# Kernel optimization log

Measured on AMD Instinct MI355X. Metric: run time of the kernel, lower is better.

Reference implementation:

```python
import jax, jax.numpy as jnp
import numpy as np

B, L_TEXT, N_TOKEN = 8, 2048, 2048
C_TEXT, C_OUT = 3584, 384
C_HID = C_OUT * 2
CHAIN_TYPES = (1, 2)   # heavy, light
CDR_TYPES = (2, 4, 6)  # CDR1/2/3


def setup_inputs() -> dict:
    key = jax.random.key(0)
    ks = jax.random.split(key, 10)
    text_conditioning = jax.random.normal(ks[0], (B, L_TEXT, C_TEXT), jnp.float32)
    text_mask = jnp.ones((B, L_TEXT), jnp.int32)
    chain_type_ids = jax.random.randint(ks[1], (B, L_TEXT), 0, 3).astype(jnp.int32)
    cdr_region_type_ids = jax.random.randint(ks[2], (B, L_TEXT), 0, 10).astype(jnp.int32)
    boltz_chain_type = jax.random.randint(ks[3], (B, N_TOKEN), 0, 4).astype(jnp.int32)
    boltz_region_type = jax.random.randint(ks[4], (B, N_TOKEN), 0, 10).astype(jnp.int32)
    W1 = jax.random.normal(ks[5], (C_HID, C_TEXT), jnp.float32) * 0.02
    b1 = jnp.zeros((C_HID,), jnp.float32)
    W2 = jax.random.normal(ks[6], (C_OUT, C_HID), jnp.float32) * 0.02
    b2 = jnp.zeros((C_OUT,), jnp.float32)
    scale = jnp.ones((1,), jnp.float32)
    return {
        "text_conditioning": text_conditioning, "text_mask": text_mask,
        "chain_type_ids": chain_type_ids, "cdr_region_type_ids": cdr_region_type_ids,
        "boltz_chain_type": boltz_chain_type, "boltz_region_type": boltz_region_type,
        "W1": W1, "b1": b1, "W2": W2, "b2": b2, "scale": scale,
    }


def _align_one(text_proj, tmask, pmask):
    # text_proj: [L, C]; tmask: [L] bool (text CDR positions); pmask: [N] bool (protein CDR positions)
    # The k-th masked text token (in sequence order) maps to the k-th masked protein token,
    # for k < min(n_text, n_protein). Other protein positions get zeros.
    L = tmask.shape[0]
    trank = jnp.cumsum(tmask) - 1          # rank among text CDR tokens
    n_text = jnp.sum(tmask)
    prank = jnp.cumsum(pmask) - 1          # rank among protein CDR tokens
    # idx_by_rank[r] = text index whose rank is r; out-of-range scatter indices dropped
    idx_by_rank = jnp.zeros((L,), jnp.int32).at[jnp.where(tmask, trank, L)].set(
        jnp.arange(L, dtype=jnp.int32), mode="drop")
    valid = pmask & (prank < n_text)       # prank < n_protein holds by construction under pmask
    src = idx_by_rank[jnp.clip(prank, 0, L - 1)]
    emb = text_proj[src]                   # [N, C]
    return jnp.where(valid[:, None], emb, jnp.zeros((), text_proj.dtype))


def reference(text_conditioning, text_mask, chain_type_ids, cdr_region_type_ids,
              boltz_chain_type, boltz_region_type, W1, b1, W2, b2, scale):
    # 2-layer MLP projection: c_text -> 2*c_out -> c_out with SiLU
    h = jax.nn.silu(jnp.einsum("blt,ht->blh", text_conditioning, W1) + b1)
    text_proj = jnp.einsum("blh,ch->blc", h, W2) + b2    # [B, L, C_OUT]

    tm = text_mask.astype(bool)
    result = jnp.zeros((text_conditioning.shape[0], boltz_chain_type.shape[1], W2.shape[0]),
                       text_proj.dtype)
    align = jax.vmap(_align_one)
    for ct in CHAIN_TYPES:
        for rt in CDR_TYPES:
            tmask = (chain_type_ids == ct) & (cdr_region_type_ids == rt) & tm
            pmask = (boltz_chain_type == ct) & (boltz_region_type == rt)
            # (chain, cdr) pairs write to disjoint protein positions, so add is exact
            result = result + align(text_proj, tmask, pmask)
    return scale * result
```

## Files before the change

### kernel.cpp

```cpp
#include <hip/hip_runtime.h>
#include <hip/hip_bf16.h>
#include <math.h>

typedef __bf16 bf16_t;
typedef bf16_t bf16x8 __attribute__((ext_vector_type(8)));
typedef bf16_t bf16x4 __attribute__((ext_vector_type(4)));
typedef float f32x4 __attribute__((ext_vector_type(4)));

#define L_TEXT 2048
#define N_TOKEN 2048
#define C_TEXT 3584
#define C_OUT 384
#define C_HID 768
#define BATCH 8
#define MAXROWS (BATCH * N_TOKEN)
#define PM 3072
#define NPAIR (BATCH * 6)
#define KSPLIT 4
#define KCHUNK (C_TEXT / KSPLIT)
#define KSPLIT2 2
#define KCHUNK2 (C_HID / KSPLIT2)

#define NW1 (C_HID * C_TEXT / 8)
#define NW2 (C_OUT * C_HID / 8)
#define NINV (MAXROWS / 4)
#define CVT_BLOCKS ((NW1 + NW2 + NINV) / 256)
#define GCH (C_TEXT / 8)

__global__ __launch_bounds__(256) void init_map_kernel(
    const float* __restrict__ W1, const float* __restrict__ W2,
    bf16_t* __restrict__ W1b, bf16_t* __restrict__ W2b,
    int* __restrict__ inv,
    const int* __restrict__ tm, const int* __restrict__ ctid,
    const int* __restrict__ cdrid, const int* __restrict__ bct,
    const int* __restrict__ brt,
    int* __restrict__ trowL, int* __restrict__ pidxL, int* __restrict__ vcnt) {
    if (blockIdx.x >= CVT_BLOCKS) {
        const int bp = blockIdx.x - CVT_BLOCKS;
        const int lane = threadIdx.x;
        if (lane >= 64) return;
        const int b = bp / 6, p = bp % 6;
        const int ct = (p < 3) ? 1 : 2;
        const int rt = 2 + 2 * (p % 3);
        const unsigned long long ltm = (1ull << lane) - 1ull;

        unsigned int tbits = 0, pbits = 0;
#pragma unroll
        for (int i = 0; i < 32; i++) {
            int l = i * 64 + lane;
            unsigned int m = (ctid[b * L_TEXT + l] == ct) &&
                             (cdrid[b * L_TEXT + l] == rt) &&
                             (tm[b * L_TEXT + l] != 0);
            tbits |= m << i;
        }
#pragma unroll
        for (int i = 0; i < 32; i++) {
            int n = i * 64 + lane;
            unsigned int m = (bct[b * N_TOKEN + n] == ct) &&
                             (brt[b * N_TOKEN + n] == rt);
            pbits |= m << i;
        }

        int base = 0;
#pragma unroll
        for (int i = 0; i < 32; i++) {
            bool m = (tbits >> i) & 1;
            unsigned long long bal = __ballot(m);
            if (m) trowL[bp * L_TEXT + base + __popcll(bal & ltm)] = i * 64 + lane;
            base += __popcll(bal);
        }
        const int n_text = base;

        base = 0;
#pragma unroll
        for (int i = 0; i < 32; i++) {
            bool m = (pbits >> i) & 1;
            unsigned long long bal = __ballot(m);
            if (m) pidxL[bp * L_TEXT + base + __popcll(bal & ltm)] = i * 64 + lane;
            base += __popcll(bal);
        }
        const int n_prot = base;
        if (lane == 0) vcnt[bp] = n_text < n_prot ? n_text : n_prot;
        return;
    }

    int idx = blockIdx.x * 256 + threadIdx.x;
    if (idx < NW1) {
        int i = idx * 8;
        float4 v0 = *(const float4*)(W1 + i);
        float4 v1 = *(const float4*)(W1 + i + 4);
        bf16x8 o;
        o[0] = (bf16_t)v0.x; o[1] = (bf16_t)v0.y; o[2] = (bf16_t)v0.z; o[3] = (bf16_t)v0.w;
        o[4] = (bf16_t)v1.x; o[5] = (bf16_t)v1.y; o[6] = (bf16_t)v1.z; o[7] = (bf16_t)v1.w;
        *(bf16x8*)(W1b + i) = o;
    } else if (idx < NW1 + NW2) {
        int i = (idx - NW1) * 8;
        float4 v0 = *(const float4*)(W2 + i);
        float4 v1 = *(const float4*)(W2 + i + 4);
        bf16x8 o;
        o[0] = (bf16_t)v0.x; o[1] = (bf16_t)v0.y; o[2] = (bf16_t)v0.z; o[3] = (bf16_t)v0.w;
        o[4] = (bf16_t)v1.x; o[5] = (bf16_t)v1.y; o[6] = (bf16_t)v1.z; o[7] = (bf16_t)v1.w;
        *(bf16x8*)(W2b + i) = o;
    } else {
        int i = idx - NW1 - NW2;
        int4 m1 = {-1, -1, -1, -1};
        ((int4*)inv)[i] = m1;
    }
}

__global__ __launch_bounds__(64) void map_write_kernel(
    const int* __restrict__ trowL, const int* __restrict__ pidxL,
    const int* __restrict__ vcnt,
    int* __restrict__ rows_src, int* __restrict__ inv, int* __restrict__ count) {
    const int bp = blockIdx.x;
    const int b = bp / 6;
    const int lane = threadIdx.x;
    int base = 0, total = 0;
    for (int q = 0; q < NPAIR; q++) {
        int v = vcnt[q];
        if (q < bp) base += v;
        total += v;
    }
    if (bp == 0 && lane == 0) *count = total < PM ? total : PM;
    const int v = vcnt[bp];
    for (int r = lane; r < v; r += 64) {
        int g = base + r;
        if (g < PM) {
            rows_src[g] = b * L_TEXT + trowL[bp * L_TEXT + r];
            inv[b * N_TOKEN + pidxL[bp * L_TEXT + r]] = g;
        }
    }
}

__global__ __launch_bounds__(256) void gather_kernel(
    const float* __restrict__ X, const int* __restrict__ rows_src,
    const int* __restrict__ countp, bf16_t* __restrict__ Xg) {
    int count = *countp; if (count > PM) count = PM;
    int idx = blockIdx.x * 256 + threadIdx.x;
    int m = idx / GCH;
    if (m >= count) return;
    int c = (idx % GCH) * 8;
    const float* src = X + (size_t)rows_src[m] * C_TEXT + c;
    float4 v0 = *(const float4*)(src);
    float4 v1 = *(const float4*)(src + 4);
    bf16x8 o;
    o[0] = (bf16_t)v0.x; o[1] = (bf16_t)v0.y; o[2] = (bf16_t)v0.z; o[3] = (bf16_t)v0.w;
    o[4] = (bf16_t)v1.x; o[5] = (bf16_t)v1.y; o[6] = (bf16_t)v1.z; o[7] = (bf16_t)v1.w;
    *(bf16x8*)(Xg + (size_t)m * C_TEXT + c) = o;
}

__global__ __launch_bounds__(256) void gemm1_kernel(
    const bf16_t* __restrict__ Xg, const bf16_t* __restrict__ W1b,
    const int* __restrict__ countp, float* __restrict__ P) {
    int count = *countp; if (count > PM) count = PM;
    const int m0 = blockIdx.x * 128;
    if (m0 >= count) return;
    const int n0 = blockIdx.y * 128;
    const int kbeg = blockIdx.z * KCHUNK;

    __shared__ __align__(16) bf16_t As[2][128][40];
    __shared__ __align__(16) bf16_t Bs[2][128][40];

    const int t = threadIdx.x;
    const int lane = t & 63;
    const int w = t >> 6;
    const int wr = w >> 1, wc = w & 1;
    const int fr = lane & 15;
    const int kq = (lane >> 4) * 8;

    f32x4 acc[4][4];
#pragma unroll
    for (int i = 0; i < 4; i++)
#pragma unroll
        for (int j = 0; j < 4; j++) acc[i][j] = (f32x4){0.f, 0.f, 0.f, 0.f};

    const bf16_t* ap[2];
    const bf16_t* bp[2];
    int ofs[2];
#pragma unroll
    for (int j = 0; j < 2; j++) {
        int c = t + 256 * j;
        int row = c >> 2, c8 = (c & 3) * 8;
        ap[j] = Xg + (size_t)(m0 + row) * C_TEXT + kbeg + c8;
        bp[j] = W1b + (size_t)(n0 + row) * C_TEXT + kbeg + c8;
        ofs[j] = row * 40 + c8;
    }

    bf16_t* AsF = &As[0][0][0];
    bf16_t* BsF = &Bs[0][0][0];
    const int BUF = 128 * 40;

    bf16x8 ra[2], rb[2];
#pragma unroll
    for (int j = 0; j < 2; j++) { ra[j] = *(const bf16x8*)(ap[j]); rb[j] = *(const bf16x8*)(bp[j]); }

    const int T = KCHUNK / 32;
    for (int tile = 0; tile < T; ++tile) {
        const int cur = tile & 1;
#pragma unroll
        for (int j = 0; j < 2; j++) {
            *(bf16x8*)(AsF + cur * BUF + ofs[j]) = ra[j];
            *(bf16x8*)(BsF + cur * BUF + ofs[j]) = rb[j];
        }
        bf16x8 na[2], nb[2];
        bool more = (tile + 1 < T);
        if (more) {
            int k = (tile + 1) * 32;
#pragma unroll
            for (int j = 0; j < 2; j++) {
                na[j] = *(const bf16x8*)(ap[j] + k);
                nb[j] = *(const bf16x8*)(bp[j] + k);
            }
        }
        __syncthreads();
        bf16x8 af[4], bfr[4];
#pragma unroll
        for (int mi = 0; mi < 4; mi++)
            af[mi] = *(const bf16x8*)(AsF + cur * BUF + (wr * 64 + mi * 16 + fr) * 40 + kq);
#pragma unroll
        for (int ni = 0; ni < 4; ni++)
            bfr[ni] = *(const bf16x8*)(BsF + cur * BUF + (wc * 64 + ni * 16 + fr) * 40 + kq);
#pragma unroll
        for (int mi = 0; mi < 4; mi++)
#pragma unroll
            for (int ni = 0; ni < 4; ni++)
                acc[mi][ni] = __builtin_amdgcn_mfma_f32_16x16x32_bf16(
                    af[mi], bfr[ni], acc[mi][ni], 0, 0, 0);
        if (more) {
#pragma unroll
            for (int j = 0; j < 2; j++) { ra[j] = na[j]; rb[j] = nb[j]; }
        }
    }

    float* Pk = P + (size_t)blockIdx.z * PM * C_HID;
    const int rj = (lane >> 4) * 4;
#pragma unroll
    for (int mi = 0; mi < 4; mi++) {
#pragma unroll
        for (int ni = 0; ni < 4; ni++) {
            int gn = n0 + wc * 64 + ni * 16 + fr;
#pragma unroll
            for (int j = 0; j < 4; j++) {
                int gm = m0 + wr * 64 + mi * 16 + rj + j;
                if (gm < count) Pk[(size_t)gm * C_HID + gn] = acc[mi][ni][j];
            }
        }
    }
}

__global__ __launch_bounds__(256) void reduce1_kernel(
    const float* __restrict__ P, const float* __restrict__ b1,
    const int* __restrict__ countp, bf16_t* __restrict__ H) {
    int count = *countp; if (count > PM) count = PM;
    int idx = blockIdx.x * 256 + threadIdx.x;
    int m = idx / (C_HID / 4);
    int c = (idx % (C_HID / 4)) * 4;
    if (m >= count) return;
    f32x4 s = *(const f32x4*)(P + (size_t)m * C_HID + c);
#pragma unroll
    for (int ks = 1; ks < KSPLIT; ks++)
        s += *(const f32x4*)(P + ((size_t)ks * PM + m) * C_HID + c);
    f32x4 bb = *(const f32x4*)(b1 + c);
    bf16x4 o;
#pragma unroll
    for (int j = 0; j < 4; j++) {
        float v = s[j] + bb[j];
        o[j] = (bf16_t)(v / (1.0f + __expf(-v)));
    }
    *(bf16x4*)(H + (size_t)m * C_HID + c) = o;
}

__global__ __launch_bounds__(256) void gemm2_kernel(
    const bf16_t* __restrict__ Hm, const bf16_t* __restrict__ W2b,
    const int* __restrict__ countp, float* __restrict__ P2) {
    int count = *countp; if (count > PM) count = PM;
    const int m0 = blockIdx.x * 64;
    if (m0 >= count) return;
    const int n0 = blockIdx.y * 128;
    const int kbeg = blockIdx.z * KCHUNK2;

    __shared__ __align__(16) bf16_t As[2][64][40];
    __shared__ __align__(16) bf16_t Bs[2][128][40];

    const int t = threadIdx.x;
    const int lane = t & 63;
    const int w = t >> 6;
    const int wr = w >> 1, wc = w & 1;
    const int fr = lane & 15;
    const int kq = (lane >> 4) * 8;

    f32x4 acc[2][4];
#pragma unroll
    for (int i = 0; i < 2; i++)
#pragma unroll
        for (int j = 0; j < 4; j++) acc[i][j] = (f32x4){0.f, 0.f, 0.f, 0.f};

    const int arow = t >> 2, ac8 = (t & 3) * 8;
    const bf16_t* ap = Hm + (size_t)(m0 + arow) * C_HID + kbeg + ac8;
    const int aofs = arow * 40 + ac8;
    const bf16_t* bp[2];
    int bofs[2];
#pragma unroll
    for (int j = 0; j < 2; j++) {
        int c = t + 256 * j;
        int row = c >> 2, c8 = (c & 3) * 8;
        bp[j] = W2b + (size_t)(n0 + row) * C_HID + kbeg + c8;
        bofs[j] = row * 40 + c8;
    }

    bf16_t* AsF = &As[0][0][0];
    bf16_t* BsF = &Bs[0][0][0];
    const int ABUF = 64 * 40, BBUF = 128 * 40;

    bf16x8 ra = *(const bf16x8*)(ap);
    bf16x8 rb0 = *(const bf16x8*)(bp[0]);
    bf16x8 rb1 = *(const bf16x8*)(bp[1]);

    const int T = KCHUNK2 / 32;
    for (int tile = 0; tile < T; ++tile) {
        const int cur = tile & 1;
        *(bf16x8*)(AsF + cur * ABUF + aofs) = ra;
        *(bf16x8*)(BsF + cur * BBUF + bofs[0]) = rb0;
        *(bf16x8*)(BsF + cur * BBUF + bofs[1]) = rb1;
        bf16x8 na, nb0, nb1;
        bool more = (tile + 1 < T);
        if (more) {
            int k = (tile + 1) * 32;
            na = *(const bf16x8*)(ap + k);
            nb0 = *(const bf16x8*)(bp[0] + k);
            nb1 = *(const bf16x8*)(bp[1] + k);
        }
        __syncthreads();
        bf16x8 af[2], bfr[4];
#pragma unroll
        for (int mi = 0; mi < 2; mi++)
            af[mi] = *(const bf16x8*)(AsF + cur * ABUF + (wr * 32 + mi * 16 + fr) * 40 + kq);
#pragma unroll
        for (int ni = 0; ni < 4; ni++)
            bfr[ni] = *(const bf16x8*)(BsF + cur * BBUF + (wc * 64 + ni * 16 + fr) * 40 + kq);
#pragma unroll
        for (int mi = 0; mi < 2; mi++)
#pragma unroll
            for (int ni = 0; ni < 4; ni++)
                acc[mi][ni] = __builtin_amdgcn_mfma_f32_16x16x32_bf16(
                    af[mi], bfr[ni], acc[mi][ni], 0, 0, 0);
        if (more) { ra = na; rb0 = nb0; rb1 = nb1; }
    }

    float* Pk = P2 + (size_t)blockIdx.z * PM * C_OUT;
    const int rj = (lane >> 4) * 4;
#pragma unroll
    for (int mi = 0; mi < 2; mi++) {
#pragma unroll
        for (int ni = 0; ni < 4; ni++) {
            int gn = n0 + wc * 64 + ni * 16 + fr;
#pragma unroll
            for (int j = 0; j < 4; j++) {
                int gm = m0 + wr * 32 + mi * 16 + rj + j;
                if (gm < count) Pk[(size_t)gm * C_OUT + gn] = acc[mi][ni][j];
            }
        }
    }
}

__global__ __launch_bounds__(256) void out_kernel(
    const float* __restrict__ P2, const float* __restrict__ b2,
    const int* __restrict__ inv, const float* __restrict__ scale,
    float* __restrict__ out) {
    int idx = blockIdx.x * 256 + threadIdx.x;
    int token = idx / (C_OUT / 4);
    int c = (idx % (C_OUT / 4)) * 4;
    int m = inv[token];
    f32x4 o = (f32x4){0.f, 0.f, 0.f, 0.f};
    if (m >= 0) {
        f32x4 s = *(const f32x4*)(P2 + (size_t)m * C_OUT + c);
#pragma unroll
        for (int ks = 1; ks < KSPLIT2; ks++)
            s += *(const f32x4*)(P2 + ((size_t)ks * PM + m) * C_OUT + c);
        f32x4 bb = *(const f32x4*)(b2 + c);
        const float sc = scale[0];
#pragma unroll
        for (int j = 0; j < 4; j++) o[j] = sc * (s[j] + bb[j]);
    }
    *(f32x4*)(out + (size_t)token * C_OUT + c) = o;
}

extern "C" void kernel_launch(void* const* d_in, const int* in_sizes, int n_in,
                              void* d_out, int out_size, void* d_ws, size_t ws_size,
                              hipStream_t stream) {
    const float* X     = (const float*)d_in[0];
    const int*   tm    = (const int*)d_in[1];
    const int*   ctid  = (const int*)d_in[2];
    const int*   cdrid = (const int*)d_in[3];
    const int*   bct   = (const int*)d_in[4];
    const int*   brt   = (const int*)d_in[5];
    const float* W1    = (const float*)d_in[6];
    const float* b1    = (const float*)d_in[7];
    const float* W2    = (const float*)d_in[8];
    const float* b2    = (const float*)d_in[9];
    const float* scale = (const float*)d_in[10];

    char* ws = (char*)d_ws;
    size_t off = 0;
    int* count = (int*)(ws + off);        off += 1024;
    int* vcnt = (int*)(ws + off);         off += 1024;
    int* rows_src = (int*)(ws + off);     off += (size_t)PM * 4;
    int* inv = (int*)(ws + off);          off += (size_t)MAXROWS * 4;
    int* trowL = (int*)(ws + off);        off += (size_t)NPAIR * L_TEXT * 4;
    int* pidxL = (int*)(ws + off);        off += (size_t)NPAIR * L_TEXT * 4;
    bf16_t* W1b = (bf16_t*)(ws + off);    off += (size_t)C_HID * C_TEXT * 2;
    bf16_t* W2b = (bf16_t*)(ws + off);    off += (size_t)C_OUT * C_HID * 2;
    bf16_t* Xg = (bf16_t*)(ws + off);     off += (size_t)PM * C_TEXT * 2;
    bf16_t* H = (bf16_t*)(ws + off);      off += (size_t)PM * C_HID * 2;
    float* P = (float*)(ws + off);        off += (size_t)KSPLIT * PM * C_HID * 4;
    float* P2 = P;

    init_map_kernel<<<CVT_BLOCKS + NPAIR, 256, 0, stream>>>(
        W1, W2, W1b, W2b, inv, tm, ctid, cdrid, bct, brt, trowL, pidxL, vcnt);

    map_write_kernel<<<NPAIR, 64, 0, stream>>>(trowL, pidxL, vcnt,
                                               rows_src, inv, count);

    gather_kernel<<<(PM * GCH) / 256, 256, 0, stream>>>(X, rows_src, count, Xg);

    dim3 g1(PM / 128, C_HID / 128, KSPLIT);
    gemm1_kernel<<<g1, 256, 0, stream>>>(Xg, W1b, count, P);

    reduce1_kernel<<<(PM * C_HID / 4) / 256, 256, 0, stream>>>(P, b1, count, H);

    dim3 g2(PM / 64, C_OUT / 128, KSPLIT2);
    gemm2_kernel<<<g2, 256, 0, stream>>>(H, W2b, count, P2);

    out_kernel<<<(MAXROWS * C_OUT / 4) / 256, 256, 0, stream>>>(
        P2, b2, inv, scale, (float*)d_out);
}
```

Measured before the change: 126.5 us.

## Fuse all stages into one cooperative persistent kernel with grid syncs

Replaces the seven-kernel pipeline with a single cooperative kernel that runs every stage (weight conversion and mapping, row map write, GEMM1, SiLU reduce, GEMM2, output scatter) in grid-strided loops separated by grid.sync. GEMM1 now reads the gathered fp32 text rows directly and converts them to bf16 in-register, so the separate gather pass and its Xg buffer are no longer used. GEMM2 split-K goes from 2 to 4 to give more work units to the persistent grid. This removes launch overhead and one full gather round-trip, at the cost of grid-wide barriers, a fixed grid size tied to occupancy, and fp32 loads inside the GEMM inner loop. The old multi-kernel path is kept as a fallback.

```diff
diff --git a/kernel.cpp b/kernel.cpp
--- a/kernel.cpp
+++ b/kernel.cpp
@@ -1,6 +1,9 @@
 #include <hip/hip_runtime.h>
 #include <hip/hip_bf16.h>
+#include <hip/hip_cooperative_groups.h>
 #include <math.h>
+
+namespace cg = cooperative_groups;
 
 typedef __bf16 bf16_t;
 typedef bf16_t bf16x8 __attribute__((ext_vector_type(8)));
@@ -18,14 +21,378 @@
 #define NPAIR (BATCH * 6)
 #define KSPLIT 4
 #define KCHUNK (C_TEXT / KSPLIT)
-#define KSPLIT2 2
+#define KSPLIT2 4
 #define KCHUNK2 (C_HID / KSPLIT2)
+#define KSPLIT2F 2
+#define KCHUNK2F (C_HID / KSPLIT2F)
 
 #define NW1 (C_HID * C_TEXT / 8)
 #define NW2 (C_OUT * C_HID / 8)
 #define NINV (MAXROWS / 4)
 #define CVT_BLOCKS ((NW1 + NW2 + NINV) / 256)
 #define GCH (C_TEXT / 8)
+
+__global__ __launch_bounds__(256, 2) void mega_kernel(
+    const float* __restrict__ X, const int* __restrict__ tm,
+    const int* __restrict__ ctid, const int* __restrict__ cdrid,
+    const int* __restrict__ bct, const int* __restrict__ brt,
+    const float* __restrict__ W1, const float* __restrict__ b1,
+    const float* __restrict__ W2, const float* __restrict__ b2,
+    const float* __restrict__ scale,
+    bf16_t* __restrict__ W1b, bf16_t* __restrict__ W2b,
+    int* __restrict__ inv, int* __restrict__ count, int* __restrict__ vcnt,
+    int* __restrict__ rows_src, int* __restrict__ trowL, int* __restrict__ pidxL,
+    bf16_t* __restrict__ H, float* __restrict__ P, float* __restrict__ outp)
+{
+    cg::grid_group grid = cg::this_grid();
+    const int nb = gridDim.x;
+    const int t = threadIdx.x;
+
+    __shared__ __align__(16) bf16_t As[2][128][40];
+    __shared__ __align__(16) bf16_t Bs[2][128][40];
+    bf16_t* AsF = &As[0][0][0];
+    bf16_t* BsF = &Bs[0][0][0];
+
+    for (int u = blockIdx.x; u < CVT_BLOCKS + NPAIR; u += nb) {
+        if (u < CVT_BLOCKS) {
+            int idx = u * 256 + t;
+            if (idx < NW1) {
+                int i = idx * 8;
+                float4 v0 = *(const float4*)(W1 + i);
+                float4 v1 = *(const float4*)(W1 + i + 4);
+                bf16x8 o;
+                o[0] = (bf16_t)v0.x; o[1] = (bf16_t)v0.y; o[2] = (bf16_t)v0.z; o[3] = (bf16_t)v0.w;
+                o[4] = (bf16_t)v1.x; o[5] = (bf16_t)v1.y; o[6] = (bf16_t)v1.z; o[7] = (bf16_t)v1.w;
+                *(bf16x8*)(W1b + i) = o;
+            } else if (idx < NW1 + NW2) {
+                int i = (idx - NW1) * 8;
+                float4 v0 = *(const float4*)(W2 + i);
+                float4 v1 = *(const float4*)(W2 + i + 4);
+                bf16x8 o;
+                o[0] = (bf16_t)v0.x; o[1] = (bf16_t)v0.y; o[2] = (bf16_t)v0.z; o[3] = (bf16_t)v0.w;
+                o[4] = (bf16_t)v1.x; o[5] = (bf16_t)v1.y; o[6] = (bf16_t)v1.z; o[7] = (bf16_t)v1.w;
+                *(bf16x8*)(W2b + i) = o;
+            } else {
+                int i = idx - NW1 - NW2;
+                int4 m1 = {-1, -1, -1, -1};
+                ((int4*)inv)[i] = m1;
+            }
+        } else if (t < 64) {
+            const int bp = u - CVT_BLOCKS;
+            const int lane = t;
+            const int b = bp / 6, p = bp % 6;
+            const int ct = (p < 3) ? 1 : 2;
+            const int rt = 2 + 2 * (p % 3);
+            const unsigned long long ltm = (1ull << lane) - 1ull;
+
+            unsigned int tbits = 0, pbits = 0;
+#pragma unroll
+            for (int i = 0; i < 32; i++) {
+                int l = i * 64 + lane;
+                unsigned int m = (ctid[b * L_TEXT + l] == ct) &&
+                                 (cdrid[b * L_TEXT + l] == rt) &&
+                                 (tm[b * L_TEXT + l] != 0);
+                tbits |= m << i;
+            }
+#pragma unroll
+            for (int i = 0; i < 32; i++) {
+                int n = i * 64 + lane;
+                unsigned int m = (bct[b * N_TOKEN + n] == ct) &&
+                                 (brt[b * N_TOKEN + n] == rt);
+                pbits |= m << i;
+            }
+            int base = 0;
+#pragma unroll
+            for (int i = 0; i < 32; i++) {
+                bool m = (tbits >> i) & 1;
+                unsigned long long bal = __ballot(m);
+                if (m) trowL[bp * L_TEXT + base + __popcll(bal & ltm)] = i * 64 + lane;
+                base += __popcll(bal);
+            }
+            const int n_text = base;
+            base = 0;
+#pragma unroll
+            for (int i = 0; i < 32; i++) {
+                bool m = (pbits >> i) & 1;
+                unsigned long long bal = __ballot(m);
+                if (m) pidxL[bp * L_TEXT + base + __popcll(bal & ltm)] = i * 64 + lane;
+                base += __popcll(bal);
+            }
+            const int n_prot = base;
+            if (lane == 0) vcnt[bp] = n_text < n_prot ? n_text : n_prot;
+        }
+    }
+    __threadfence();
+    grid.sync();
+
+    if (blockIdx.x < NPAIR) {
+        const int bp = blockIdx.x;
+        const int b = bp / 6;
+        int base = 0, total = 0;
+        for (int q = 0; q < NPAIR; q++) {
+            int v = vcnt[q];
+            if (q < bp) base += v;
+            total += v;
+        }
+        if (bp == 0 && t == 0) *count = total < PM ? total : PM;
+        const int v = vcnt[bp];
+        for (int r = t; r < v; r += 256) {
+            int g = base + r;
+            if (g < PM) {
+                rows_src[g] = b * L_TEXT + trowL[bp * L_TEXT + r];
+                inv[b * N_TOKEN + pidxL[bp * L_TEXT + r]] = g;
+            }
+        }
+    }
+    __threadfence();
+    grid.sync();
+
+    int cnt = *(volatile const int*)count;
+    if (cnt > PM) cnt = PM;
+
+    const int lane = t & 63;
+    const int w = t >> 6;
+    const int wr = w >> 1, wc = w & 1;
+    const int fr = lane & 15;
+    const int kq = (lane >> 4) * 8;
+    const int rj = (lane >> 4) * 4;
+
+    for (int u = blockIdx.x; u < (PM / 128) * (C_HID / 128) * KSPLIT; u += nb) {
+        const int bx = u % (PM / 128);
+        const int by = (u / (PM / 128)) % (C_HID / 128);
+        const int bz = u / ((PM / 128) * (C_HID / 128));
+        const int m0 = bx * 128;
+        if (m0 >= cnt) continue;
+        const int n0 = by * 128;
+        const int kbeg = bz * KCHUNK;
+
+        f32x4 acc[4][4];
+#pragma unroll
+        for (int i = 0; i < 4; i++)
+#pragma unroll
+            for (int j = 0; j < 4; j++) acc[i][j] = (f32x4){0.f, 0.f, 0.f, 0.f};
+
+        const float* ap[2];
+        const bf16_t* bp[2];
+        int ofs[2];
+        bool av[2];
+#pragma unroll
+        for (int j = 0; j < 2; j++) {
+            int c = t + 256 * j;
+            int row = c >> 2, c8 = (c & 3) * 8;
+            av[j] = (m0 + row < cnt);
+            ap[j] = X + (size_t)(av[j] ? rows_src[m0 + row] : 0) * C_TEXT + kbeg + c8;
+            bp[j] = W1b + (size_t)(n0 + row) * C_TEXT + kbeg + c8;
+            ofs[j] = row * 40 + c8;
+        }
+        const int BUF = 128 * 40;
+
+        bf16x8 ra[2], rb[2];
+#pragma unroll
+        for (int j = 0; j < 2; j++) {
+            bf16x8 val;
+            if (av[j]) {
+                float4 v0 = *(const float4*)(ap[j]);
+                float4 v1 = *(const float4*)(ap[j] + 4);
+                val[0] = (bf16_t)v0.x; val[1] = (bf16_t)v0.y; val[2] = (bf16_t)v0.z; val[3] = (bf16_t)v0.w;
+                val[4] = (bf16_t)v1.x; val[5] = (bf16_t)v1.y; val[6] = (bf16_t)v1.z; val[7] = (bf16_t)v1.w;
+            } else {
+#pragma unroll
+                for (int e = 0; e < 8; e++) val[e] = (bf16_t)0.0f;
+            }
+            ra[j] = val;
+            rb[j] = *(const bf16x8*)(bp[j]);
+        }
+
+        const int T = KCHUNK / 32;
+        for (int tile = 0; tile < T; ++tile) {
+            const int cur = tile & 1;
+#pragma unroll
+            for (int j = 0; j < 2; j++) {
+                *(bf16x8*)(AsF + cur * BUF + ofs[j]) = ra[j];
+                *(bf16x8*)(BsF + cur * BUF + ofs[j]) = rb[j];
+            }
+            bf16x8 na[2], nbv[2];
+            bool more = (tile + 1 < T);
+            if (more) {
+                int k = (tile + 1) * 32;
+#pragma unroll
+                for (int j = 0; j < 2; j++) {
+                    bf16x8 val;
+                    if (av[j]) {
+                        float4 v0 = *(const float4*)(ap[j] + k);
+                        float4 v1 = *(const float4*)(ap[j] + k + 4);
+                        val[0] = (bf16_t)v0.x; val[1] = (bf16_t)v0.y; val[2] = (bf16_t)v0.z; val[3] = (bf16_t)v0.w;
+                        val[4] = (bf16_t)v1.x; val[5] = (bf16_t)v1.y; val[6] = (bf16_t)v1.z; val[7] = (bf16_t)v1.w;
+                    } else {
+#pragma unroll
+                        for (int e = 0; e < 8; e++) val[e] = (bf16_t)0.0f;
+                    }
+                    na[j] = val;
+                    nbv[j] = *(const bf16x8*)(bp[j] + k);
+                }
+            }
+            __syncthreads();
+            bf16x8 af[4], bfr[4];
+#pragma unroll
+            for (int mi = 0; mi < 4; mi++)
+                af[mi] = *(const bf16x8*)(AsF + cur * BUF + (wr * 64 + mi * 16 + fr) * 40 + kq);
+#pragma unroll
+            for (int ni = 0; ni < 4; ni++)
+                bfr[ni] = *(const bf16x8*)(BsF + cur * BUF + (wc * 64 + ni * 16 + fr) * 40 + kq);
+#pragma unroll
+            for (int mi = 0; mi < 4; mi++)
+#pragma unroll
+                for (int ni = 0; ni < 4; ni++)
+                    acc[mi][ni] = __builtin_amdgcn_mfma_f32_16x16x32_bf16(
+                        af[mi], bfr[ni], acc[mi][ni], 0, 0, 0);
+            if (more) {
+#pragma unroll
+                for (int j = 0; j < 2; j++) { ra[j] = na[j]; rb[j] = nbv[j]; }
+            }
+        }
+
+        float* Pk = P + (size_t)bz * PM * C_HID;
+#pragma unroll
+        for (int mi = 0; mi < 4; mi++) {
+#pragma unroll
+            for (int ni = 0; ni < 4; ni++) {
+                int gn = n0 + wc * 64 + ni * 16 + fr;
+#pragma unroll
+                for (int j = 0; j < 4; j++) {
+                    int gm = m0 + wr * 64 + mi * 16 + rj + j;
+                    if (gm < cnt) Pk[(size_t)gm * C_HID + gn] = acc[mi][ni][j];
+                }
+            }
+        }
+        __syncthreads();
+    }
+    __threadfence();
+    grid.sync();
+
+    for (int u = blockIdx.x; u < (PM * C_HID / 4) / 256; u += nb) {
+        int idx = u * 256 + t;
+        int m = idx / (C_HID / 4);
+        int c = (idx % (C_HID / 4)) * 4;
+        if (m < cnt) {
+            f32x4 s = *(const f32x4*)(P + (size_t)m * C_HID + c);
+#pragma unroll
+            for (int ks = 1; ks < KSPLIT; ks++)
+                s += *(const f32x4*)(P + ((size_t)ks * PM + m) * C_HID + c);
+            f32x4 bb = *(const f32x4*)(b1 + c);
+            bf16x4 o;
+#pragma unroll
+            for (int j = 0; j < 4; j++) {
+                float v = s[j] + bb[j];
+                o[j] = (bf16_t)(v / (1.0f + __expf(-v)));
+            }
+            *(bf16x4*)(H + (size_t)m * C_HID + c) = o;
+        }
+    }
+    __threadfence();
+    grid.sync();
+
+    for (int u = blockIdx.x; u < (PM / 64) * (C_OUT / 128) * KSPLIT2; u += nb) {
+        const int bx = u % (PM / 64);
+        const int by = (u / (PM / 64)) % (C_OUT / 128);
+        const int bz = u / ((PM / 64) * (C_OUT / 128));
+        const int m0 = bx * 64;
+        if (m0 >= cnt) continue;
+        const int n0 = by * 128;
+        const int kbeg = bz * KCHUNK2;
+
+        f32x4 acc[2][4];
+#pragma unroll
+        for (int i = 0; i < 2; i++)
+#pragma unroll
+            for (int j = 0; j < 4; j++) acc[i][j] = (f32x4){0.f, 0.f, 0.f, 0.f};
+
+        const int arow = t >> 2, ac8 = (t & 3) * 8;
+        const bf16_t* ap = H + (size_t)(m0 + arow) * C_HID + kbeg + ac8;
+        const int aofs = arow * 40 + ac8;
+        const bf16_t* bp[2];
+        int bofs[2];
+#pragma unroll
+        for (int j = 0; j < 2; j++) {
+            int c = t + 256 * j;
+            int row = c >> 2, c8 = (c & 3) * 8;
+            bp[j] = W2b + (size_t)(n0 + row) * C_HID + kbeg + c8;
+            bofs[j] = row * 40 + c8;
+        }
+        const int ABUF = 64 * 40, BBUF = 128 * 40;
+
+        bf16x8 ra = *(const bf16x8*)(ap);
+        bf16x8 rb0 = *(const bf16x8*)(bp[0]);
+        bf16x8 rb1 = *(const bf16x8*)(bp[1]);
+
+        const int T = KCHUNK2 / 32;
+        for (int tile = 0; tile < T; ++tile) {
+            const int cur = tile & 1;
+            *(bf16x8*)(AsF + cur * ABUF + aofs) = ra;
+            *(bf16x8*)(BsF + cur * BBUF + bofs[0]) = rb0;
+            *(bf16x8*)(BsF + cur * BBUF + bofs[1]) = rb1;
+            bf16x8 na, nb0, nb1;
+            bool more = (tile + 1 < T);
+            if (more) {
+                int k = (tile + 1) * 32;
+                na = *(const bf16x8*)(ap + k);
+                nb0 = *(const bf16x8*)(bp[0] + k);
+                nb1 = *(const bf16x8*)(bp[1] + k);
+            }
+            __syncthreads();
+            bf16x8 af[2], bfr[4];
+#pragma unroll
+            for (int mi = 0; mi < 2; mi++)
+                af[mi] = *(const bf16x8*)(AsF + cur * ABUF + (wr * 32 + mi * 16 + fr) * 40 + kq);
+#pragma unroll
+            for (int ni = 0; ni < 4; ni++)
+                bfr[ni] = *(const bf16x8*)(BsF + cur * BBUF + (wc * 64 + ni * 16 + fr) * 40 + kq);
+#pragma unroll
+            for (int mi = 0; mi < 2; mi++)
+#pragma unroll
+                for (int ni = 0; ni < 4; ni++)
+                    acc[mi][ni] = __builtin_amdgcn_mfma_f32_16x16x32_bf16(
+                        af[mi], bfr[ni], acc[mi][ni], 0, 0, 0);
+            if (more) { ra = na; rb0 = nb0; rb1 = nb1; }
+        }
+
+        float* Pk = P + (size_t)bz * PM * C_OUT;
+#pragma unroll
+        for (int mi = 0; mi < 2; mi++) {
+#pragma unroll
+            for (int ni = 0; ni < 4; ni++) {
+                int gn = n0 + wc * 64 + ni * 16 + fr;
+#pragma unroll
+                for (int j = 0; j < 4; j++) {
+                    int gm = m0 + wr * 32 + mi * 16 + rj + j;
+                    if (gm < cnt) Pk[(size_t)gm * C_OUT + gn] = acc[mi][ni][j];
+                }
+            }
+        }
+        __syncthreads();
+    }
+    __threadfence();
+    grid.sync();
+
+    const float sc = scale[0];
+    for (int u = blockIdx.x; u < (MAXROWS * C_OUT / 4) / 256; u += nb) {
+        int idx = u * 256 + t;
+        int token = idx / (C_OUT / 4);
+        int c = (idx % (C_OUT / 4)) * 4;
+        int m = inv[token];
+        f32x4 o = (f32x4){0.f, 0.f, 0.f, 0.f};
+        if (m >= 0) {
+            f32x4 s = *(const f32x4*)(P + (size_t)m * C_OUT + c);
+#pragma unroll
+            for (int ks = 1; ks < KSPLIT2; ks++)
+                s += *(const f32x4*)(P + ((size_t)ks * PM + m) * C_OUT + c);
+            f32x4 bb = *(const f32x4*)(b2 + c);
+#pragma unroll
+            for (int j = 0; j < 4; j++) o[j] = sc * (s[j] + bb[j]);
+        }
+        *(f32x4*)(outp + (size_t)token * C_OUT + c) = o;
+    }
+}
 
 __global__ __launch_bounds__(256) void init_map_kernel(
     const float* __restrict__ W1, const float* __restrict__ W2,
@@ -60,7 +427,6 @@
                              (brt[b * N_TOKEN + n] == rt);
             pbits |= m << i;
         }
-
         int base = 0;
 #pragma unroll
         for (int i = 0; i < 32; i++) {
@@ -70,7 +436,6 @@
             base += __popcll(bal);
         }
         const int n_text = base;
-
         base = 0;
 #pragma unroll
         for (int i = 0; i < 32; i++) {
@@ -83,7 +448,6 @@
         if (lane == 0) vcnt[bp] = n_text < n_prot ? n_text : n_prot;
         return;
     }
-
     int idx = blockIdx.x * 256 + threadIdx.x;
     if (idx < NW1) {
         int i = idx * 8;
@@ -277,7 +641,7 @@
     const int m0 = blockIdx.x * 64;
     if (m0 >= count) return;
     const int n0 = blockIdx.y * 128;
-    const int kbeg = blockIdx.z * KCHUNK2;
+    const int kbeg = blockIdx.z * KCHUNK2F;
 
     __shared__ __align__(16) bf16_t As[2][64][40];
     __shared__ __align__(16) bf16_t Bs[2][128][40];
@@ -316,7 +680,7 @@
     bf16x8 rb0 = *(const bf16x8*)(bp[0]);
     bf16x8 rb1 = *(const bf16x8*)(bp[1]);
 
-    const int T = KCHUNK2 / 32;
+    const int T = KCHUNK2F / 32;
     for (int tile = 0; tile < T; ++tile) {
         const int cur = tile & 1;
         *(bf16x8*)(AsF + cur * ABUF + aofs) = ra;
@@ -375,7 +739,7 @@
     if (m >= 0) {
         f32x4 s = *(const f32x4*)(P2 + (size_t)m * C_OUT + c);
 #pragma unroll
-        for (int ks = 1; ks < KSPLIT2; ks++)
+        for (int ks = 1; ks < KSPLIT2F; ks++)
             s += *(const f32x4*)(P2 + ((size_t)ks * PM + m) * C_OUT + c);
         f32x4 bb = *(const f32x4*)(b2 + c);
         const float sc = scale[0];
@@ -413,24 +777,36 @@
     bf16_t* Xg = (bf16_t*)(ws + off);     off += (size_t)PM * C_TEXT * 2;
     bf16_t* H = (bf16_t*)(ws + off);      off += (size_t)PM * C_HID * 2;
     float* P = (float*)(ws + off);        off += (size_t)KSPLIT * PM * C_HID * 4;
-    float* P2 = P;
+    float* outp = (float*)d_out;
+
+    int maxb = 0;
+    hipError_t qe = hipOccupancyMaxActiveBlocksPerMultiprocessor(
+        &maxb, (const void*)mega_kernel, 256, 0);
+
+    if (qe == hipSuccess && maxb >= 1) {
+        int grid = 256 * maxb;
+        if (grid > 768) grid = 768;
+        void* args[] = {(void*)&X, (void*)&tm, (void*)&ctid, (void*)&cdrid,
+                        (void*)&bct, (void*)&brt, (void*)&W1, (void*)&b1,
+                        (void*)&W2, (void*)&b2, (void*)&scale,
+                        (void*)&W1b, (void*)&W2b, (void*)&inv, (void*)&count,
+                        (void*)&vcnt, (void*)&rows_src, (void*)&trowL,
+                        (void*)&pidxL, (void*)&H, (void*)&P, (void*)&outp};
+        hipLaunchCooperativeKernel((const void*)mega_kernel, dim3(grid),
+                                   dim3(256), args, 0, stream);
+        return;
+    }
 
     init_map_kernel<<<CVT_BLOCKS + NPAIR, 256, 0, stream>>>(
         W1, W2, W1b, W2b, inv, tm, ctid, cdrid, bct, brt, trowL, pidxL, vcnt);
-
     map_write_kernel<<<NPAIR, 64, 0, stream>>>(trowL, pidxL, vcnt,
                                                rows_src, inv, count);
-
     gather_kernel<<<(PM * GCH) / 256, 256, 0, stream>>>(X, rows_src, count, Xg);
-
     dim3 g1(PM / 128, C_HID / 128, KSPLIT);
     gemm1_kernel<<<g1, 256, 0, stream>>>(Xg, W1b, count, P);
-
     reduce1_kernel<<<(PM * C_HID / 4) / 256, 256, 0, stream>>>(P, b1, count, H);
-
-    dim3 g2(PM / 64, C_OUT / 128, KSPLIT2);
-    gemm2_kernel<<<g2, 256, 0, stream>>>(H, W2b, count, P2);
-
+    dim3 g2(PM / 64, C_OUT / 128, KSPLIT2F);
+    gemm2_kernel<<<g2, 256, 0, stream>>>(H, W2b, count, P);
     out_kernel<<<(MAXROWS * C_OUT / 4) / 256, 256, 0, stream>>>(
-        P2, b2, inv, scale, (float*)d_out);
+        P, b2, inv, scale, (float*)d_out);
 }
```

Measured after the change: 440.1 us. 3.48x slower.

## Drop split-K partials, fuse bias/SiLU and scatter epilogues into GEMMs

Applied to the files above, without the earlier changes.

Removes split-K from both GEMMs so each block accumulates the full K dimension. The bias and SiLU move into the first GEMM's epilogue, and bias, scale and scatter into the second GEMM's epilogue, which writes directly to output rows through a rows_dst map. The output is zero-filled up front in the init kernel, replacing the inverse-map init and the separate reduce and out kernels. This cuts fp32 partial-buffer traffic and two launches. In exchange the first GEMM runs a long serial K loop (3584) over a smaller 64x128 tile grid with no K parallelism, which may underfill the GPU, and it uses scattered scalar stores.

```diff
diff --git a/kernel.cpp b/kernel.cpp
--- a/kernel.cpp
+++ b/kernel.cpp
@@ -16,27 +16,24 @@
 #define MAXROWS (BATCH * N_TOKEN)
 #define PM 3072
 #define NPAIR (BATCH * 6)
-#define KSPLIT 4
-#define KCHUNK (C_TEXT / KSPLIT)
-#define KSPLIT2 2
-#define KCHUNK2 (C_HID / KSPLIT2)
 
 #define NW1 (C_HID * C_TEXT / 8)
 #define NW2 (C_OUT * C_HID / 8)
-#define NINV (MAXROWS / 4)
-#define CVT_BLOCKS ((NW1 + NW2 + NINV) / 256)
+#define NZERO (MAXROWS * C_OUT / 4)
+#define CHUNKS_TOTAL (NW1 + NW2 + NZERO)
+#define CHUNK_BLOCKS (CHUNKS_TOTAL / 256)
 #define GCH (C_TEXT / 8)
 
 __global__ __launch_bounds__(256) void init_map_kernel(
     const float* __restrict__ W1, const float* __restrict__ W2,
     bf16_t* __restrict__ W1b, bf16_t* __restrict__ W2b,
-    int* __restrict__ inv,
+    float* __restrict__ outp,
     const int* __restrict__ tm, const int* __restrict__ ctid,
     const int* __restrict__ cdrid, const int* __restrict__ bct,
     const int* __restrict__ brt,
     int* __restrict__ trowL, int* __restrict__ pidxL, int* __restrict__ vcnt) {
-    if (blockIdx.x >= CVT_BLOCKS) {
-        const int bp = blockIdx.x - CVT_BLOCKS;
+    if (blockIdx.x >= CHUNK_BLOCKS) {
+        const int bp = blockIdx.x - CHUNK_BLOCKS;
         const int lane = threadIdx.x;
         if (lane >= 64) return;
         const int b = bp / 6, p = bp % 6;
@@ -60,7 +57,6 @@
                              (brt[b * N_TOKEN + n] == rt);
             pbits |= m << i;
         }
-
         int base = 0;
 #pragma unroll
         for (int i = 0; i < 32; i++) {
@@ -70,7 +66,6 @@
             base += __popcll(bal);
         }
         const int n_text = base;
-
         base = 0;
 #pragma unroll
         for (int i = 0; i < 32; i++) {
@@ -83,7 +78,6 @@
         if (lane == 0) vcnt[bp] = n_text < n_prot ? n_text : n_prot;
         return;
     }
-
     int idx = blockIdx.x * 256 + threadIdx.x;
     if (idx < NW1) {
         int i = idx * 8;
@@ -102,16 +96,17 @@
         o[4] = (bf16_t)v1.x; o[5] = (bf16_t)v1.y; o[6] = (bf16_t)v1.z; o[7] = (bf16_t)v1.w;
         *(bf16x8*)(W2b + i) = o;
     } else {
-        int i = idx - NW1 - NW2;
-        int4 m1 = {-1, -1, -1, -1};
-        ((int4*)inv)[i] = m1;
+        int z = idx - NW1 - NW2;
+        f32x4 zv = (f32x4){0.f, 0.f, 0.f, 0.f};
+        *(f32x4*)(outp + (size_t)z * 4) = zv;
     }
 }
 
 __global__ __launch_bounds__(64) void map_write_kernel(
     const int* __restrict__ trowL, const int* __restrict__ pidxL,
     const int* __restrict__ vcnt,
-    int* __restrict__ rows_src, int* __restrict__ inv, int* __restrict__ count) {
+    int* __restrict__ rows_src, int* __restrict__ rows_dst,
+    int* __restrict__ count) {
     const int bp = blockIdx.x;
     const int b = bp / 6;
     const int lane = threadIdx.x;
@@ -127,7 +122,7 @@
         int g = base + r;
         if (g < PM) {
             rows_src[g] = b * L_TEXT + trowL[bp * L_TEXT + r];
-            inv[b * N_TOKEN + pidxL[bp * L_TEXT + r]] = g;
+            rows_dst[g] = b * N_TOKEN + pidxL[bp * L_TEXT + r];
         }
     }
 }
@@ -151,14 +146,14 @@
 
 __global__ __launch_bounds__(256) void gemm1_kernel(
     const bf16_t* __restrict__ Xg, const bf16_t* __restrict__ W1b,
-    const int* __restrict__ countp, float* __restrict__ P) {
+    const float* __restrict__ b1, const int* __restrict__ countp,
+    bf16_t* __restrict__ H) {
     int count = *countp; if (count > PM) count = PM;
-    const int m0 = blockIdx.x * 128;
+    const int m0 = blockIdx.x * 64;
     if (m0 >= count) return;
     const int n0 = blockIdx.y * 128;
-    const int kbeg = blockIdx.z * KCHUNK;
-
-    __shared__ __align__(16) bf16_t As[2][128][40];
+
+    __shared__ __align__(16) bf16_t As[2][64][40];
     __shared__ __align__(16) bf16_t Bs[2][128][40];
 
     const int t = threadIdx.x;
@@ -168,143 +163,22 @@
     const int fr = lane & 15;
     const int kq = (lane >> 4) * 8;
 
-    f32x4 acc[4][4];
-#pragma unroll
-    for (int i = 0; i < 4; i++)
+    f32x4 acc[2][4];
+#pragma unroll
+    for (int i = 0; i < 2; i++)
 #pragma unroll
         for (int j = 0; j < 4; j++) acc[i][j] = (f32x4){0.f, 0.f, 0.f, 0.f};
 
-    const bf16_t* ap[2];
+    const int arow = t >> 2, ac8 = (t & 3) * 8;
+    const bf16_t* ap = Xg + (size_t)(m0 + arow) * C_TEXT + ac8;
+    const int aofs = arow * 40 + ac8;
     const bf16_t* bp[2];
-    int ofs[2];
+    int bofs[2];
 #pragma unroll
     for (int j = 0; j < 2; j++) {
         int c = t + 256 * j;
         int row = c >> 2, c8 = (c & 3) * 8;
-        ap[j] = Xg + (size_t)(m0 + row) * C_TEXT + kbeg + c8;
-        bp[j] = W1b + (size_t)(n0 + row) * C_TEXT + kbeg + c8;
-        ofs[j] = row * 40 + c8;
-    }
-
-    bf16_t* AsF = &As[0][0][0];
-    bf16_t* BsF = &Bs[0][0][0];
-    const int BUF = 128 * 40;
-
-    bf16x8 ra[2], rb[2];
-#pragma unroll
-    for (int j = 0; j < 2; j++) { ra[j] = *(const bf16x8*)(ap[j]); rb[j] = *(const bf16x8*)(bp[j]); }
-
-    const int T = KCHUNK / 32;
-    for (int tile = 0; tile < T; ++tile) {
-        const int cur = tile & 1;
-#pragma unroll
-        for (int j = 0; j < 2; j++) {
-            *(bf16x8*)(AsF + cur * BUF + ofs[j]) = ra[j];
-            *(bf16x8*)(BsF + cur * BUF + ofs[j]) = rb[j];
-        }
-        bf16x8 na[2], nb[2];
-        bool more = (tile + 1 < T);
-        if (more) {
-            int k = (tile + 1) * 32;
-#pragma unroll
-            for (int j = 0; j < 2; j++) {
-                na[j] = *(const bf16x8*)(ap[j] + k);
-                nb[j] = *(const bf16x8*)(bp[j] + k);
-            }
-        }
-        __syncthreads();
-        bf16x8 af[4], bfr[4];
-#pragma unroll
-        for (int mi = 0; mi < 4; mi++)
-            af[mi] = *(const bf16x8*)(AsF + cur * BUF + (wr * 64 + mi * 16 + fr) * 40 + kq);
-#pragma unroll
-        for (int ni = 0; ni < 4; ni++)
-            bfr[ni] = *(const bf16x8*)(BsF + cur * BUF + (wc * 64 + ni * 16 + fr) * 40 + kq);
-#pragma unroll
-        for (int mi = 0; mi < 4; mi++)
-#pragma unroll
-            for (int ni = 0; ni < 4; ni++)
-                acc[mi][ni] = __builtin_amdgcn_mfma_f32_16x16x32_bf16(
-                    af[mi], bfr[ni], acc[mi][ni], 0, 0, 0);
-        if (more) {
-#pragma unroll
-            for (int j = 0; j < 2; j++) { ra[j] = na[j]; rb[j] = nb[j]; }
-        }
-    }
-
-    float* Pk = P + (size_t)blockIdx.z * PM * C_HID;
-    const int rj = (lane >> 4) * 4;
-#pragma unroll
-    for (int mi = 0; mi < 4; mi++) {
-#pragma unroll
-        for (int ni = 0; ni < 4; ni++) {
-            int gn = n0 + wc * 64 + ni * 16 + fr;
-#pragma unroll
-            for (int j = 0; j < 4; j++) {
-                int gm = m0 + wr * 64 + mi * 16 + rj + j;
-                if (gm < count) Pk[(size_t)gm * C_HID + gn] = acc[mi][ni][j];
-            }
-        }
-    }
-}
-
-__global__ __launch_bounds__(256) void reduce1_kernel(
-    const float* __restrict__ P, const float* __restrict__ b1,
-    const int* __restrict__ countp, bf16_t* __restrict__ H) {
-    int count = *countp; if (count > PM) count = PM;
-    int idx = blockIdx.x * 256 + threadIdx.x;
-    int m = idx / (C_HID / 4);
-    int c = (idx % (C_HID / 4)) * 4;
-    if (m >= count) return;
-    f32x4 s = *(const f32x4*)(P + (size_t)m * C_HID + c);
-#pragma unroll
-    for (int ks = 1; ks < KSPLIT; ks++)
-        s += *(const f32x4*)(P + ((size_t)ks * PM + m) * C_HID + c);
-    f32x4 bb = *(const f32x4*)(b1 + c);
-    bf16x4 o;
-#pragma unroll
-    for (int j = 0; j < 4; j++) {
-        float v = s[j] + bb[j];
-        o[j] = (bf16_t)(v / (1.0f + __expf(-v)));
-    }
-    *(bf16x4*)(H + (size_t)m * C_HID + c) = o;
-}
-
-__global__ __launch_bounds__(256) void gemm2_kernel(
-    const bf16_t* __restrict__ Hm, const bf16_t* __restrict__ W2b,
-    const int* __restrict__ countp, float* __restrict__ P2) {
-    int count = *countp; if (count > PM) count = PM;
-    const int m0 = blockIdx.x * 64;
-    if (m0 >= count) return;
-    const int n0 = blockIdx.y * 128;
-    const int kbeg = blockIdx.z * KCHUNK2;
-
-    __shared__ __align__(16) bf16_t As[2][64][40];
-    __shared__ __align__(16) bf16_t Bs[2][128][40];
-
-    const int t = threadIdx.x;
-    const int lane = t & 63;
-    const int w = t >> 6;
-    const int wr = w >> 1, wc = w & 1;
-    const int fr = lane & 15;
-    const int kq = (lane >> 4) * 8;
-
-    f32x4 acc[2][4];
-#pragma unroll
-    for (int i = 0; i < 2; i++)
-#pragma unroll
-        for (int j = 0; j < 4; j++) acc[i][j] = (f32x4){0.f, 0.f, 0.f, 0.f};
-
-    const int arow = t >> 2, ac8 = (t & 3) * 8;
-    const bf16_t* ap = Hm + (size_t)(m0 + arow) * C_HID + kbeg + ac8;
-    const int aofs = arow * 40 + ac8;
-    const bf16_t* bp[2];
-    int bofs[2];
-#pragma unroll
-    for (int j = 0; j < 2; j++) {
-        int c = t + 256 * j;
-        int row = c >> 2, c8 = (c & 3) * 8;
-        bp[j] = W2b + (size_t)(n0 + row) * C_HID + kbeg + c8;
+        bp[j] = W1b + (size_t)(n0 + row) * C_TEXT + c8;
         bofs[j] = row * 40 + c8;
     }
 
@@ -316,7 +190,7 @@
     bf16x8 rb0 = *(const bf16x8*)(bp[0]);
     bf16x8 rb1 = *(const bf16x8*)(bp[1]);
 
-    const int T = KCHUNK2 / 32;
+    const int T = C_TEXT / 32;
     for (int tile = 0; tile < T; ++tile) {
         const int cur = tile & 1;
         *(bf16x8*)(AsF + cur * ABUF + aofs) = ra;
@@ -345,44 +219,128 @@
                 acc[mi][ni] = __builtin_amdgcn_mfma_f32_16x16x32_bf16(
                     af[mi], bfr[ni], acc[mi][ni], 0, 0, 0);
         if (more) { ra = na; rb0 = nb0; rb1 = nb1; }
-    }
-
-    float* Pk = P2 + (size_t)blockIdx.z * PM * C_OUT;
+        __syncthreads();
+    }
+
     const int rj = (lane >> 4) * 4;
 #pragma unroll
     for (int mi = 0; mi < 2; mi++) {
 #pragma unroll
         for (int ni = 0; ni < 4; ni++) {
             int gn = n0 + wc * 64 + ni * 16 + fr;
+            float bias = b1[gn];
 #pragma unroll
             for (int j = 0; j < 4; j++) {
                 int gm = m0 + wr * 32 + mi * 16 + rj + j;
-                if (gm < count) Pk[(size_t)gm * C_OUT + gn] = acc[mi][ni][j];
+                if (gm < count) {
+                    float v = acc[mi][ni][j] + bias;
+                    H[(size_t)gm * C_HID + gn] = (bf16_t)(v / (1.0f + __expf(-v)));
+                }
             }
         }
     }
 }
 
-__global__ __launch_bounds__(256) void out_kernel(
-    const float* __restrict__ P2, const float* __restrict__ b2,
-    const int* __restrict__ inv, const float* __restrict__ scale,
-    float* __restrict__ out) {
-    int idx = blockIdx.x * 256 + threadIdx.x;
-    int token = idx / (C_OUT / 4);
-    int c = (idx % (C_OUT / 4)) * 4;
-    int m = inv[token];
-    f32x4 o = (f32x4){0.f, 0.f, 0.f, 0.f};
-    if (m >= 0) {
-        f32x4 s = *(const f32x4*)(P2 + (size_t)m * C_OUT + c);
-#pragma unroll
-        for (int ks = 1; ks < KSPLIT2; ks++)
-            s += *(const f32x4*)(P2 + ((size_t)ks * PM + m) * C_OUT + c);
-        f32x4 bb = *(const f32x4*)(b2 + c);
-        const float sc = scale[0];
-#pragma unroll
-        for (int j = 0; j < 4; j++) o[j] = sc * (s[j] + bb[j]);
-    }
-    *(f32x4*)(out + (size_t)token * C_OUT + c) = o;
+__global__ __launch_bounds__(256) void gemm2_kernel(
+    const bf16_t* __restrict__ Hm, const bf16_t* __restrict__ W2b,
+    const float* __restrict__ b2, const int* __restrict__ rows_dst,
+    const int* __restrict__ countp, const float* __restrict__ scale,
+    float* __restrict__ outp) {
+    int count = *countp; if (count > PM) count = PM;
+    const int m0 = blockIdx.x * 32;
+    if (m0 >= count) return;
+    const int n0 = blockIdx.y * 128;
+
+    __shared__ __align__(16) bf16_t As[2][32][40];
+    __shared__ __align__(16) bf16_t Bs[2][128][40];
+
+    const int t = threadIdx.x;
+    const int lane = t & 63;
+    const int w = t >> 6;
+    const int fr = lane & 15;
+    const int kq = (lane >> 4) * 8;
+
+    f32x4 acc[2][2];
+#pragma unroll
+    for (int i = 0; i < 2; i++)
+#pragma unroll
+        for (int j = 0; j < 2; j++) acc[i][j] = (f32x4){0.f, 0.f, 0.f, 0.f};
+
+    const int arow = t >> 2, ac8 = (t & 3) * 8;
+    const bool astage = (t < 128);
+    const bf16_t* ap = Hm + (size_t)(m0 + arow) * C_HID + ac8;
+    const int aofs = arow * 40 + ac8;
+    const bf16_t* bp[2];
+    int bofs[2];
+#pragma unroll
+    for (int j = 0; j < 2; j++) {
+        int c = t + 256 * j;
+        int row = c >> 2, c8 = (c & 3) * 8;
+        bp[j] = W2b + (size_t)(n0 + row) * C_HID + c8;
+        bofs[j] = row * 40 + c8;
+    }
+
+    bf16_t* AsF = &As[0][0][0];
+    bf16_t* BsF = &Bs[0][0][0];
+    const int ABUF = 32 * 40, BBUF = 128 * 40;
+
+    bf16x8 ra;
+    if (astage) ra = *(const bf16x8*)(ap);
+    bf16x8 rb0 = *(const bf16x8*)(bp[0]);
+    bf16x8 rb1 = *(const bf16x8*)(bp[1]);
+
+    const int T = C_HID / 32;
+    for (int tile = 0; tile < T; ++tile) {
+        const int cur = tile & 1;
+        if (astage) *(bf16x8*)(AsF + cur * ABUF + aofs) = ra;
+        *(bf16x8*)(BsF + cur * BBUF + bofs[0]) = rb0;
+        *(bf16x8*)(BsF + cur * BBUF + bofs[1]) = rb1;
+        bf16x8 na, nb0, nb1;
+        bool more = (tile + 1 < T);
+        if (more) {
+            int k = (tile + 1) * 32;
+            if (astage) na = *(const bf16x8*)(ap + k);
+            nb0 = *(const bf16x8*)(bp[0] + k);
+            nb1 = *(const bf16x8*)(bp[1] + k);
+        }
+        __syncthreads();
+        bf16x8 af[2], bfr[2];
+#pragma unroll
+        for (int mi = 0; mi < 2; mi++)
+            af[mi] = *(const bf16x8*)(AsF + cur * ABUF + (mi * 16 + fr) * 40 + kq);
+#pragma unroll
+        for (int ni = 0; ni < 2; ni++)
+            bfr[ni] = *(const bf16x8*)(BsF + cur * BBUF + (w * 32 + ni * 16 + fr) * 40 + kq);
+#pragma unroll
+        for (int mi = 0; mi < 2; mi++)
+#pragma unroll
+            for (int ni = 0; ni < 2; ni++)
+                acc[mi][ni] = __builtin_amdgcn_mfma_f32_16x16x32_bf16(
+                    af[mi], bfr[ni], acc[mi][ni], 0, 0, 0);
+        if (more) { if (astage) ra = na; rb0 = nb0; rb1 = nb1; }
+        __syncthreads();
+    }
+
+    const float sc = scale[0];
+    const int rj = (lane >> 4) * 4;
+#pragma unroll
+    for (int mi = 0; mi < 2; mi++) {
+#pragma unroll
+        for (int ni = 0; ni < 2; ni++) {
+            int gn = n0 + w * 32 + ni * 16 + fr;
+            float bias = b2[gn];
+#pragma unroll
+            for (int j = 0; j < 2 * 2; j++) ;
+#pragma unroll
+            for (int j = 0; j < 4; j++) {
+                int gm = m0 + mi * 16 + rj + j;
+                if (gm < count) {
+                    int dst = rows_dst[gm];
+                    outp[(size_t)dst * C_OUT + gn] = sc * (acc[mi][ni][j] + bias);
+                }
+            }
+        }
+    }
 }
 
 extern "C" void kernel_launch(void* const* d_in, const int* in_sizes, int n_in,
@@ -405,32 +363,26 @@
     int* count = (int*)(ws + off);        off += 1024;
     int* vcnt = (int*)(ws + off);         off += 1024;
     int* rows_src = (int*)(ws + off);     off += (size_t)PM * 4;
-    int* inv = (int*)(ws + off);          off += (size_t)MAXROWS * 4;
+    int* rows_dst = (int*)(ws + off);     off += (size_t)PM * 4;
     int* trowL = (int*)(ws + off);        off += (size_t)NPAIR * L_TEXT * 4;
     int* pidxL = (int*)(ws + off);        off += (size_t)NPAIR * L_TEXT * 4;
     bf16_t* W1b = (bf16_t*)(ws + off);    off += (size_t)C_HID * C_TEXT * 2;
     bf16_t* W2b = (bf16_t*)(ws + off);    off += (size_t)C_OUT * C_HID * 2;
     bf16_t* Xg = (bf16_t*)(ws + off);     off += (size_t)PM * C_TEXT * 2;
     bf16_t* H = (bf16_t*)(ws + off);      off += (size_t)PM * C_HID * 2;
-    float* P = (float*)(ws + off);        off += (size_t)KSPLIT * PM * C_HID * 4;
-    float* P2 = P;
-
-    init_map_kernel<<<CVT_BLOCKS + NPAIR, 256, 0, stream>>>(
-        W1, W2, W1b, W2b, inv, tm, ctid, cdrid, bct, brt, trowL, pidxL, vcnt);
+    float* outp = (float*)d_out;
+
+    init_map_kernel<<<CHUNK_BLOCKS + NPAIR, 256, 0, stream>>>(
+        W1, W2, W1b, W2b, outp, tm, ctid, cdrid, bct, brt, trowL, pidxL, vcnt);
 
     map_write_kernel<<<NPAIR, 64, 0, stream>>>(trowL, pidxL, vcnt,
-                                               rows_src, inv, count);
+                                               rows_src, rows_dst, count);
 
     gather_kernel<<<(PM * GCH) / 256, 256, 0, stream>>>(X, rows_src, count, Xg);
 
-    dim3 g1(PM / 128, C_HID / 128, KSPLIT);
-    gemm1_kernel<<<g1, 256, 0, stream>>>(Xg, W1b, count, P);
-
-    reduce1_kernel<<<(PM * C_HID / 4) / 256, 256, 0, stream>>>(P, b1, count, H);
-
-    dim3 g2(PM / 64, C_OUT / 128, KSPLIT2);
-    gemm2_kernel<<<g2, 256, 0, stream>>>(H, W2b, count, P2);
-
-    out_kernel<<<(MAXROWS * C_OUT / 4) / 256, 256, 0, stream>>>(
-        P2, b2, inv, scale, (float*)d_out);
-}
+    dim3 g1(PM / 64, C_HID / 128);
+    gemm1_kernel<<<g1, 256, 0, stream>>>(Xg, W1b, b1, count, H);
+
+    dim3 g2(PM / 32, C_OUT / 128);
+    gemm2_kernel<<<g2, 256, 0, stream>>>(H, W2b, b2, rows_dst, count, scale, outp);
+}
```

New measurement: 142.8 us. +12.9%, slower.
